# Kernel tuning notes

Measured on AMD Instinct MI355X. Metric: run time of the kernel, lower is better.

## Reference

```python
import jax, jax.numpy as jnp
import numpy as np
from jax import lax

B, T, IN, H, L, K = 2048, 192, 24, 64, 2, 20


def setup_inputs() -> dict:
    key = jax.random.key(0)
    ks = jax.random.split(key, 16)
    s = 1.0 / np.sqrt(H)

    def u(k, shape):
        return jax.random.uniform(k, shape, jnp.float32, -s, s)

    # PyTorch LSTM init + forget-gate bias filled with 1.0 (bias[n//4:n//2])
    b_ih0 = u(ks[2], (4 * H,)).at[H:2 * H].set(1.0)
    b_hh0 = u(ks[3], (4 * H,)).at[H:2 * H].set(1.0)
    b_ih1 = u(ks[6], (4 * H,)).at[H:2 * H].set(1.0)
    b_hh1 = u(ks[7], (4 * H,)).at[H:2 * H].set(1.0)
    return {
        "train_batch": jax.random.normal(ks[0], (B, T, IN), jnp.float32),
        "labels_batch": jax.random.uniform(ks[1], (B, T), jnp.float32),
        "w_ih0": u(ks[4], (4 * H, IN)), "w_hh0": u(ks[5], (4 * H, H)),
        "b_ih0": b_ih0, "b_hh0": b_hh0,
        "w_ih1": u(ks[8], (4 * H, H)), "w_hh1": u(ks[9], (4 * H, H)),
        "b_ih1": b_ih1, "b_hh1": b_hh1,
        "w_b0": u(ks[10], (1, H * L)), "bb_b0": u(ks[11], (1,)),
        "w_g": u(ks[12], (K, H * L)), "b_g": u(ks[13], (K,)),
    }


def _cell(x, h, c, w_ih, w_hh, b_ih, b_hh):
    g = x @ w_ih.T + b_ih + h @ w_hh.T + b_hh
    i, f, gg, o = jnp.split(g, 4, axis=-1)  # PyTorch gate order i,f,g,o
    c2 = jax.nn.sigmoid(f) * c + jax.nn.sigmoid(i) * jnp.tanh(gg)
    h2 = jax.nn.sigmoid(o) * jnp.tanh(c2)
    return h2, c2


def _crps(beta0, gamma, labels):
    # beta0 [T,B,1], gamma [T,B,K], labels [T,B] -> per-timestep mean CRPS [T]
    Kk = gamma.shape[-1]
    b0 = beta0[..., 0]
    sig = 1.0 / Kk
    # beta = diff of (gamma - prev)/(2*sigma), with beta[...,0] seeded by beta_0
    bp = jnp.concatenate([beta0, gamma[..., :-1]], axis=-1)
    b = (gamma - bp) / (2.0 * sig)
    b = b - jnp.concatenate([jnp.zeros_like(b[..., :1]), b[..., :-1]], axis=-1)
    b = jnp.concatenate(
        [b[..., :-1], gamma[..., -1:] - b[..., :-1].sum(-1, keepdims=True)], axis=-1)
    # left knot positions ksi = [0, 1/K, ..., (K-1)/K] (via cumsum for fidelity)
    ksi_full = jnp.cumsum(jnp.full((Kk,), sig, gamma.dtype))
    ksi = jnp.concatenate([jnp.zeros((1,), gamma.dtype), ksi_full[:-1]])
    Mkk = jnp.maximum(ksi[:, None] - ksi[None, :], 0.0) ** 2  # [K,K]
    # knot values = Q(ksi): spline quantile function at left knots
    knots = b0[..., None] * ksi + jnp.einsum('tbj,ij->tbi', b, Mkk)
    diff = labels[..., None] - knots
    al = (diff > 0).astype(gamma.dtype)
    A = (al * b).sum(-1)
    Bq = b0 - 2.0 * (al * b * ksi).sum(-1)
    C = -labels + (al * b * ksi * ksi).sum(-1)
    disc = Bq * Bq - 4.0 * A * C
    ksi_pick = ksi[jnp.argmin(jnp.abs(diff), axis=-1)]
    A_safe = jnp.where(A != 0, A, 1.0)
    B_safe = jnp.where(Bq != 0, Bq, 1.0)
    quad = (-Bq + jnp.sqrt(jnp.maximum(disc, 0.0))) / (2.0 * A_safe)
    alpha = jnp.where((A != 0) & (disc >= 0), quad,
                      jnp.where(A == 0, -C / B_safe, ksi_pick))
    c1 = labels * (2.0 * alpha - 1.0)
    c2 = b0 * (1.0 / 3.0 - alpha ** 2)
    c3 = (b / 6.0 * (1.0 - ksi) ** 4).sum(-1)
    c4 = (al * (2.0 / 3.0) * b * (alpha[..., None] - ksi) ** 3).sum(-1)
    return (c1 + c2 + c3 - c4).mean(-1)  # mean over batch, per t


def reference(train_batch, labels_batch, w_ih0, w_hh0, b_ih0, b_hh0,
              w_ih1, w_hh1, b_ih1, b_hh1, w_b0, bb_b0, w_g, b_g):
    Bb = train_batch.shape[0]
    Hh = w_hh0.shape[1]
    x_seq = jnp.transpose(train_batch, (1, 0, 2))  # [T,B,IN]
    labels = labels_batch.T                         # [T,B]
    z = jnp.zeros((Bb, Hh), train_batch.dtype)

    def step(carry, x):
        h0, c0, h1, c1 = carry
        nh0, nc0 = _cell(x, h0, c0, w_ih0, w_hh0, b_ih0, b_hh0)
        nh1, nc1 = _cell(nh0, h1, c1, w_ih1, w_hh1, b_ih1, b_hh1)
        return (nh0, nc0, nh1, nc1), jnp.stack([nh0, nh1])  # [L,B,H]

    _, hs = lax.scan(step, (z, z, z, z), x_seq)  # [T,L,B,H]
    # hidden.permute(1,2,0).reshape(B, H*L): feature layout is h-major, layer-minor
    feats = jnp.transpose(hs, (0, 2, 3, 1)).reshape(hs.shape[0], Bb, Hh * L)
    beta0 = jax.nn.softplus(feats @ w_b0.T + bb_b0)  # [T,B,1]
    gamma = jax.nn.softplus(feats @ w_g.T + b_g)     # [T,B,K]
    return _crps(beta0, gamma, labels).sum()  # sum over t of per-step mean CRPS
```

## Files before the change

### kernel.cpp

```cpp
#include <hip/hip_runtime.h>
#include <math.h>

namespace {

constexpr int TT  = 192;
constexpr int INp = 24;
constexpr int Kk  = 20;
constexpr int BB  = 8;
constexpr int NTHR = 512;

constexpr int XSTR = 2308;
constexpr int HP   = 36;
constexpr int GS   = 33;

constexpr int WSA_U = 256 * 48;
constexpr int WSB_U = 256 * 64;
constexpr int WP_U  = 21 * 64;
constexpr int WTOT  = WSA_U + WSB_U + WP_U;
constexpr size_t OFF_WSB  = 49152;
constexpr size_t OFF_WP   = 114688;
constexpr size_t OFF_PART = 120832;
constexpr size_t OFF_HIST = 131072;
constexpr size_t ROW_BYTES = (size_t)TT * 64 * 4;

using short8 = __attribute__((ext_vector_type(8))) short;
using f32x4  = __attribute__((ext_vector_type(4))) float;

__device__ __forceinline__ float sigmoidf_(float x) {
  return 1.0f / (1.0f + __expf(-x));
}
__device__ __forceinline__ float tanhf_(float x) {
  return 2.0f / (1.0f + __expf(-2.0f * x)) - 1.0f;
}
__device__ __forceinline__ float softplusf_(float x) {
  return fmaxf(x, 0.0f) + log1pf(__expf(-fabsf(x)));
}
__device__ __forceinline__ unsigned cvt_pk_bf16(float a, float b) {
  unsigned r;
  asm("v_cvt_pk_bf16_f32 %0, %1, %2" : "=v"(r) : "v"(a), "v"(b));
  return r;
}
__device__ __forceinline__ unsigned bf16rne(float x) {
  unsigned u = __float_as_uint(x);
  return (u + 0x7FFFu + ((u >> 16) & 1u)) >> 16;
}
__device__ __forceinline__ short8 as_bf(uint4 u) {
  short8 s; __builtin_memcpy(&s, &u, 16); return s;
}
#define DOT2(acc, wv, vv) \
  asm("v_dot2_f32_bf16 %0, %1, %2, %0" : "+v"(acc) : "v"(wv), "v"(vv))

#define WAVE_LDS_FENCE()                                  \
  do {                                                    \
    asm volatile("s_waitcnt lgkmcnt(0)" ::: "memory");    \
    __builtin_amdgcn_sched_barrier(0);                    \
  } while (0)

__global__ void wconv_kernel(const float* __restrict__ w_ih0,
                             const float* __restrict__ w_hh0,
                             const float* __restrict__ w_ih1,
                             const float* __restrict__ w_hh1,
                             const float* __restrict__ w_b0,
                             const float* __restrict__ w_g,
                             unsigned* __restrict__ wsA,
                             unsigned* __restrict__ wsB,
                             unsigned* __restrict__ wp) {
  int i = (int)(blockIdx.x * 256 + threadIdx.x);
  if (i >= WTOT) return;
  float lo = 0.f, hi = 0.f;
  if (i < WSA_U) {
    int g = i / 48, j = i % 48;
    int orig = (g & 3) * 64 + (g >> 2);
    if (j < 12)      { lo = w_ih0[orig * 24 + 2 * j]; hi = w_ih0[orig * 24 + 2 * j + 1]; }
    else if (j < 44) { lo = w_hh0[orig * 64 + 2 * (j - 12)]; hi = w_hh0[orig * 64 + 2 * (j - 12) + 1]; }
    wsA[i] = bf16rne(lo) | (bf16rne(hi) << 16);
  } else if (i < WSA_U + WSB_U) {
    int i2 = i - WSA_U;
    int g = i2 / 64, j = i2 % 64;
    int orig = (g & 3) * 64 + (g >> 2);
    if (j < 32) { lo = w_ih1[orig * 64 + 2 * j]; hi = w_ih1[orig * 64 + 2 * j + 1]; }
    else        { lo = w_hh1[orig * 64 + 2 * (j - 32)]; hi = w_hh1[orig * 64 + 2 * (j - 32) + 1]; }
    wsB[i2] = bf16rne(lo) | (bf16rne(hi) << 16);
  } else {
    int i3 = i - WSA_U - WSB_U;
    int o = i3 >> 6, j = i3 & 63;
    const float* row = (o == 0) ? w_b0 : (w_g + (size_t)(o - 1) * 128);
    if (j < 32) { lo = row[4 * j];            hi = row[4 * j + 2]; }
    else        { lo = row[4 * (j - 32) + 1]; hi = row[4 * (j - 32) + 3]; }
    wp[i3] = bf16rne(lo) | (bf16rne(hi) << 16);
  }
}

__global__ __launch_bounds__(NTHR, 1) void lstm_kernel(
    const float* __restrict__ train,
    const float* __restrict__ b_ih0, const float* __restrict__ b_hh0,
    const float* __restrict__ b_ih1, const float* __restrict__ b_hh1,
    const unsigned* __restrict__ wsA,
    const unsigned* __restrict__ wsB,
    unsigned* __restrict__ hist,
    int rb)
{
  __shared__ __align__(16) unsigned xpk_l[BB][XSTR];
  __shared__ __align__(16) unsigned hpk0_l[2][BB][HP];
  __shared__ __align__(16) unsigned hpk1_l[2][BB][HP];
  __shared__ float gscr_l[8][BB][GS];

  const int tid   = (int)threadIdx.x;
  const int lane  = tid & 63;
  const int w     = tid >> 6;
  const int l15   = lane & 15;
  const int grp   = lane >> 4;
  const int row_a = lane & 7;
  const int crow  = lane & 7;
  const int cfl   = lane >> 3;
  const int feat  = w * 8 + cfl;
  const int r0g   = rb + (int)blockIdx.x * BB;

  for (int i = tid; i < BB * TT * 12; i += NTHR) {
    int r = i / (TT * 12), rem = i % (TT * 12);
    int t = rem / 12, u = rem % 12;
    const float* p = train + ((size_t)(r0g + r) * TT + t) * INp + 2 * u;
    float2 v = *(const float2*)p;
    xpk_l[r][t * 12 + u] = cvt_pk_bf16(v.x, v.y);
  }
  for (int i = tid; i < 2 * BB * HP; i += NTHR) {
    (&hpk0_l[0][0][0])[i] = 0u;
    (&hpk1_l[0][0][0])[i] = 0u;
  }

  uint4 wAf[2][3], wBf[2][4];
#pragma unroll
  for (int n = 0; n < 2; ++n) {
    const int gcol = w * 32 + n * 16 + l15;
    const unsigned* pa = wsA + (size_t)gcol * 48 + grp * 4;
    wAf[n][0] = *(const uint4*)(pa);
    wAf[n][1] = *(const uint4*)(pa + 16);
    wAf[n][2] = *(const uint4*)(pa + 32);
    const unsigned* pb = wsB + (size_t)gcol * 64 + grp * 4;
#pragma unroll
    for (int c = 0; c < 4; ++c) wBf[n][c] = *(const uint4*)(pb + c * 16);
  }

  float bq0[4], bq1[4];
#pragma unroll
  for (int q = 0; q < 4; ++q) {
    bq0[q] = b_ih0[q * 64 + feat] + b_hh0[q * 64 + feat];
    bq1[q] = b_ih1[q * 64 + feat] + b_hh1[q * 64 + feat];
  }
  float c0 = 0.0f, c1 = 0.0f;

  unsigned* histp = hist + (size_t)((size_t)blockIdx.x * BB + crow) * TT * 64;
  const int j0 = w * 4 + (cfl >> 1);
  const bool writer = ((cfl & 1) == 0);

  __syncthreads();

  for (int t = 0; t < TT; ++t) {
    const int wp_ = t & 1, rp_ = wp_ ^ 1;

    {
      const unsigned* p0 = (grp < 3) ? &xpk_l[row_a][t * 12 + grp * 4]
                                     : &hpk0_l[rp_][row_a][0];
      short8 A0 = as_bf(*(const uint4*)p0);
      short8 A1 = as_bf(*(const uint4*)&hpk0_l[rp_][row_a][4 + grp * 4]);
      short8 A2 = as_bf(*(const uint4*)&hpk0_l[rp_][row_a][20 + grp * 4]);
      f32x4 acc0 = {0.f, 0.f, 0.f, 0.f};
      f32x4 acc1 = {0.f, 0.f, 0.f, 0.f};
      acc0 = __builtin_amdgcn_mfma_f32_16x16x32_bf16(A0, as_bf(wAf[0][0]), acc0, 0, 0, 0);
      acc1 = __builtin_amdgcn_mfma_f32_16x16x32_bf16(A0, as_bf(wAf[1][0]), acc1, 0, 0, 0);
      acc0 = __builtin_amdgcn_mfma_f32_16x16x32_bf16(A1, as_bf(wAf[0][1]), acc0, 0, 0, 0);
      acc1 = __builtin_amdgcn_mfma_f32_16x16x32_bf16(A1, as_bf(wAf[1][1]), acc1, 0, 0, 0);
      acc0 = __builtin_amdgcn_mfma_f32_16x16x32_bf16(A2, as_bf(wAf[0][2]), acc0, 0, 0, 0);
      acc1 = __builtin_amdgcn_mfma_f32_16x16x32_bf16(A2, as_bf(wAf[1][2]), acc1, 0, 0, 0);
      if (lane < 32) {
        const int rbse = (lane >> 4) * 4;
#pragma unroll
        for (int r = 0; r < 4; ++r) {
          gscr_l[w][rbse + r][l15]      = acc0[r];
          gscr_l[w][rbse + r][l15 + 16] = acc1[r];
        }
      }
    }
    WAVE_LDS_FENCE();
    {
      float gi_ = gscr_l[w][crow][cfl * 4 + 0] + bq0[0];
      float gf_ = gscr_l[w][crow][cfl * 4 + 1] + bq0[1];
      float gg_ = gscr_l[w][crow][cfl * 4 + 2] + bq0[2];
      float go_ = gscr_l[w][crow][cfl * 4 + 3] + bq0[3];
      float cn = sigmoidf_(gf_) * c0 + sigmoidf_(gi_) * tanhf_(gg_);
      c0 = cn;
      float h0v = sigmoidf_(go_) * tanhf_(cn);
      float hpart = __shfl_xor(h0v, 8, 64);
      if (writer) {
        unsigned pk = cvt_pk_bf16(h0v, hpart);
        hpk0_l[wp_][crow][j0] = pk;
        histp[(size_t)t * 64 + j0] = pk;
      }
    }
    __syncthreads();

    {
      short8 B0 = as_bf(*(const uint4*)&hpk0_l[wp_][row_a][grp * 4]);
      short8 B1v = as_bf(*(const uint4*)&hpk0_l[wp_][row_a][16 + grp * 4]);
      short8 B2v = as_bf(*(const uint4*)&hpk1_l[rp_][row_a][grp * 4]);
      short8 B3v = as_bf(*(const uint4*)&hpk1_l[rp_][row_a][16 + grp * 4]);
      f32x4 acc0 = {0.f, 0.f, 0.f, 0.f};
      f32x4 acc1 = {0.f, 0.f, 0.f, 0.f};
      acc0 = __builtin_amdgcn_mfma_f32_16x16x32_bf16(B0, as_bf(wBf[0][0]), acc0, 0, 0, 0);
      acc1 = __builtin_amdgcn_mfma_f32_16x16x32_bf16(B0, as_bf(wBf[1][0]), acc1, 0, 0, 0);
      acc0 = __builtin_amdgcn_mfma_f32_16x16x32_bf16(B1v, as_bf(wBf[0][1]), acc0, 0, 0, 0);
      acc1 = __builtin_amdgcn_mfma_f32_16x16x32_bf16(B1v, as_bf(wBf[1][1]), acc1, 0, 0, 0);
      acc0 = __builtin_amdgcn_mfma_f32_16x16x32_bf16(B2v, as_bf(wBf[0][2]), acc0, 0, 0, 0);
      acc1 = __builtin_amdgcn_mfma_f32_16x16x32_bf16(B2v, as_bf(wBf[1][2]), acc1, 0, 0, 0);
      acc0 = __builtin_amdgcn_mfma_f32_16x16x32_bf16(B3v, as_bf(wBf[0][3]), acc0, 0, 0, 0);
      acc1 = __builtin_amdgcn_mfma_f32_16x16x32_bf16(B3v, as_bf(wBf[1][3]), acc1, 0, 0, 0);
      if (lane < 32) {
        const int rbse = (lane >> 4) * 4;
#pragma unroll
        for (int r = 0; r < 4; ++r) {
          gscr_l[w][rbse + r][l15]      = acc0[r];
          gscr_l[w][rbse + r][l15 + 16] = acc1[r];
        }
      }
    }
    WAVE_LDS_FENCE();
    {
      float gi_ = gscr_l[w][crow][cfl * 4 + 0] + bq1[0];
      float gf_ = gscr_l[w][crow][cfl * 4 + 1] + bq1[1];
      float gg_ = gscr_l[w][crow][cfl * 4 + 2] + bq1[2];
      float go_ = gscr_l[w][crow][cfl * 4 + 3] + bq1[3];
      float cn = sigmoidf_(gf_) * c1 + sigmoidf_(gi_) * tanhf_(gg_);
      c1 = cn;
      float h1v = sigmoidf_(go_) * tanhf_(cn);
      float hpart = __shfl_xor(h1v, 8, 64);
      if (writer) {
        unsigned pk = cvt_pk_bf16(h1v, hpart);
        hpk1_l[wp_][crow][j0] = pk;
        histp[(size_t)t * 64 + 32 + j0] = pk;
      }
    }
  }
}

__global__ __launch_bounds__(192, 2) void crps_kernel(
    const unsigned* __restrict__ hist,
    const float* __restrict__ labels,
    const unsigned* __restrict__ wp,
    const float* __restrict__ bb_b0,
    const float* __restrict__ b_g,
    float* __restrict__ partials,
    int rb)
{
  __shared__ unsigned wp_l[21][64];
  __shared__ float pb_l[21];
  __shared__ float rw_l[3];

  const int tid = (int)threadIdx.x;
  const int bloc = (int)blockIdx.x;
  const int bglob = rb + bloc;
  const float sig = 1.0f / (float)Kk;

  for (int i = tid; i < 21 * 64; i += 192) wp_l[i >> 6][i & 63] = wp[i];
  if (tid < 21) pb_l[tid] = (tid == 0) ? bb_b0[0] : b_g[tid - 1];
  __syncthreads();

  uint4 hh[16];
  const uint4* hp4 = (const uint4*)(hist + ((size_t)bloc * TT + tid) * 64);
#pragma unroll
  for (int c = 0; c < 16; ++c) hh[c] = hp4[c];
  const float y = labels[(size_t)bglob * TT + tid];

  float bg[21];
#pragma unroll
  for (int o = 0; o < 21; ++o) {
    float lin = pb_l[o];
#pragma unroll
    for (int c = 0; c < 16; ++c) {
      uint4 wv = *(const uint4*)&wp_l[o][c * 4];
      DOT2(lin, wv.x, hh[c].x);
      DOT2(lin, wv.y, hh[c].y);
      DOT2(lin, wv.z, hh[c].z);
      DOT2(lin, wv.w, hh[c].w);
    }
    bg[o] = softplusf_(lin);
  }

  float braw[Kk], bj[Kk], ksi[Kk];
  {
    float kv = 0.0f;
#pragma unroll
    for (int l = 0; l < Kk; ++l) { ksi[l] = kv; kv += sig; }
  }
#pragma unroll
  for (int l = 0; l < Kk; ++l) {
    float bp = (l == 0) ? bg[0] : bg[l];
    braw[l] = (bg[l + 1] - bp) / (2.0f * sig);
  }
#pragma unroll
  for (int l = 0; l < Kk; ++l)
    bj[l] = braw[l] - ((l == 0) ? 0.0f : braw[l - 1]);
  {
    float st = 0.0f;
#pragma unroll
    for (int l = 0; l < Kk - 1; ++l) st += bj[l];
    bj[Kk - 1] = bg[Kk] - st;
  }

  float A = 0.f, tB = 0.f, tC = 0.f, c3a = 0.f;
  float ab[Kk];
  float ad = 3.4e38f, kpick = 0.f;
#pragma unroll
  for (int i = 0; i < Kk; ++i) {
    float kn = bg[0] * ksi[i];
#pragma unroll
    for (int j = 0; j < Kk; ++j) {
      if (j < i) {
        float d = ksi[i] - ksi[j];
        kn = fmaf(bj[j] * d, d, kn);
      }
    }
    float diff = y - kn;
    float abv = (diff > 0.0f) ? bj[i] : 0.0f;
    ab[i] = abv;
    A += abv;
    tB = fmaf(abv, ksi[i], tB);
    tC = fmaf(abv * ksi[i], ksi[i], tC);
    float um = 1.0f - ksi[i], um2 = um * um;
    c3a = fmaf(bj[i] * (1.0f / 6.0f), um2 * um2, c3a);
    float adi = fabsf(diff);
    if (adi < ad) { ad = adi; kpick = ksi[i]; }
  }
  float Bq = bg[0] - 2.0f * tB;
  float Cc = -y + tC;
  float disc = Bq * Bq - 4.0f * A * Cc;
  float A_safe = (A != 0.0f) ? A : 1.0f;
  float B_safe = (Bq != 0.0f) ? Bq : 1.0f;
  float quad = (-Bq + sqrtf(fmaxf(disc, 0.0f))) / (2.0f * A_safe);
  float alpha = (A != 0.0f && disc >= 0.0f)
                    ? quad
                    : ((A == 0.0f) ? (-Cc / B_safe) : kpick);
  float c4 = 0.0f;
#pragma unroll
  for (int i = 0; i < Kk; ++i) {
    float d = alpha - ksi[i];
    c4 = fmaf(ab[i] * (2.0f / 3.0f), d * d * d, c4);
  }
  float crps = y * (2.0f * alpha - 1.0f) +
               bg[0] * ((1.0f / 3.0f) - alpha * alpha) + c3a - c4;

  float v = crps;
#pragma unroll
  for (int off = 32; off > 0; off >>= 1) v += __shfl_xor(v, off, 64);
  if ((tid & 63) == 0) rw_l[tid >> 6] = v;
  __syncthreads();
  if (tid == 0) partials[bglob] = rw_l[0] + rw_l[1] + rw_l[2];
}

__global__ void final_reduce_kernel(const float* __restrict__ partials,
                                    float* __restrict__ out) {
  __shared__ float s_l[1024];
  const int tid = (int)threadIdx.x;
  s_l[tid] = partials[tid] + partials[tid + 1024];
  __syncthreads();
  for (int s = 512; s > 0; s >>= 1) {
    if (tid < s) s_l[tid] += s_l[tid + s];
    __syncthreads();
  }
  if (tid == 0) out[0] = s_l[0] * (1.0f / 2048.0f);
}

}

extern "C" void kernel_launch(void* const* d_in, const int* in_sizes, int n_in,
                              void* d_out, int out_size, void* d_ws, size_t ws_size,
                              hipStream_t stream) {
  (void)in_sizes; (void)n_in; (void)out_size;
  const float* train  = (const float*)d_in[0];
  const float* labels = (const float*)d_in[1];
  const float* w_ih0  = (const float*)d_in[2];
  const float* w_hh0  = (const float*)d_in[3];
  const float* b_ih0  = (const float*)d_in[4];
  const float* b_hh0  = (const float*)d_in[5];
  const float* w_ih1  = (const float*)d_in[6];
  const float* w_hh1  = (const float*)d_in[7];
  const float* b_ih1  = (const float*)d_in[8];
  const float* b_hh1  = (const float*)d_in[9];
  const float* w_b0   = (const float*)d_in[10];
  const float* bb_b0  = (const float*)d_in[11];
  const float* w_g    = (const float*)d_in[12];
  const float* b_g    = (const float*)d_in[13];

  unsigned* wsA   = (unsigned*)d_ws;
  unsigned* wsB   = (unsigned*)((char*)d_ws + OFF_WSB);
  unsigned* wp    = (unsigned*)((char*)d_ws + OFF_WP);
  float* partials = (float*)((char*)d_ws + OFF_PART);
  unsigned* hist  = (unsigned*)((char*)d_ws + OFF_HIST);

  size_t avail = (ws_size > OFF_HIST) ? (ws_size - OFF_HIST) : 0;
  size_t rows_fit = avail / ROW_BYTES;
  int chunk = (rows_fit >= 2048) ? 2048 : (int)rows_fit;
  chunk &= ~7;
  if (chunk < 8) chunk = 8;

  wconv_kernel<<<dim3((WTOT + 255) / 256), dim3(256), 0, stream>>>(
      w_ih0, w_hh0, w_ih1, w_hh1, w_b0, w_g, wsA, wsB, wp);

  for (int rb = 0; rb < 2048; rb += chunk) {
    int cur = (2048 - rb < chunk) ? (2048 - rb) : chunk;
    lstm_kernel<<<dim3(cur / 8), dim3(NTHR), 0, stream>>>(
        train, b_ih0, b_hh0, b_ih1, b_hh1, wsA, wsB, hist, rb);
    crps_kernel<<<dim3(cur), dim3(192), 0, stream>>>(
        hist, labels, wp, bb_b0, b_g, partials, rb);
  }
  final_reduce_kernel<<<dim3(1), dim3(1024), 0, stream>>>(partials,
                                                          (float*)d_out);
}
```

Baseline: 315.2 us.

## Split LSTM gate columns across 16 waves with one MFMA tile each

```diff
diff --git a/kernel.cpp b/kernel.cpp
--- a/kernel.cpp
+++ b/kernel.cpp
@@ -7,11 +7,11 @@
 constexpr int INp = 24;
 constexpr int Kk  = 20;
 constexpr int BB  = 8;
-constexpr int NTHR = 512;
+constexpr int NTHR = 1024;
 
 constexpr int XSTR = 2308;
 constexpr int HP   = 36;
-constexpr int GS   = 33;
+constexpr int GS   = 17;
 
 constexpr int WSA_U = 256 * 48;
 constexpr int WSB_U = 256 * 64;
@@ -53,6 +53,14 @@
 #define WAVE_LDS_FENCE()                                  \
   do {                                                    \
     asm volatile("s_waitcnt lgkmcnt(0)" ::: "memory");    \
+    __builtin_amdgcn_sched_barrier(0);                    \
+  } while (0)
+
+#define BLOCK_BARRIER_LGKM()                              \
+  do {                                                    \
+    __builtin_amdgcn_sched_barrier(0);                    \
+    asm volatile("s_waitcnt lgkmcnt(0)" ::: "memory");    \
+    __builtin_amdgcn_s_barrier();                         \
     __builtin_amdgcn_sched_barrier(0);                    \
   } while (0)
 
@@ -91,7 +99,7 @@
   }
 }
 
-__global__ __launch_bounds__(NTHR, 1) void lstm_kernel(
+__global__ __launch_bounds__(NTHR, 4) void lstm_kernel(
     const float* __restrict__ train,
     const float* __restrict__ b_ih0, const float* __restrict__ b_hh0,
     const float* __restrict__ b_ih1, const float* __restrict__ b_hh1,
@@ -103,7 +111,7 @@
   __shared__ __align__(16) unsigned xpk_l[BB][XSTR];
   __shared__ __align__(16) unsigned hpk0_l[2][BB][HP];
   __shared__ __align__(16) unsigned hpk1_l[2][BB][HP];
-  __shared__ float gscr_l[8][BB][GS];
+  __shared__ float gscr_l[16][BB][GS];
 
   const int tid   = (int)threadIdx.x;
   const int lane  = tid & 63;
@@ -112,8 +120,8 @@
   const int grp   = lane >> 4;
   const int row_a = lane & 7;
   const int crow  = lane & 7;
-  const int cfl   = lane >> 3;
-  const int feat  = w * 8 + cfl;
+  const int cfl   = (lane >> 3) & 3;
+  const int feat  = w * 4 + cfl;
   const int r0g   = rb + (int)blockIdx.x * BB;
 
   for (int i = tid; i < BB * TT * 12; i += NTHR) {
@@ -128,17 +136,16 @@
     (&hpk1_l[0][0][0])[i] = 0u;
   }
 
-  uint4 wAf[2][3], wBf[2][4];
-#pragma unroll
-  for (int n = 0; n < 2; ++n) {
-    const int gcol = w * 32 + n * 16 + l15;
+  uint4 wAf[3], wBf[4];
+  {
+    const int gcol = w * 16 + l15;
     const unsigned* pa = wsA + (size_t)gcol * 48 + grp * 4;
-    wAf[n][0] = *(const uint4*)(pa);
-    wAf[n][1] = *(const uint4*)(pa + 16);
-    wAf[n][2] = *(const uint4*)(pa + 32);
+    wAf[0] = *(const uint4*)(pa);
+    wAf[1] = *(const uint4*)(pa + 16);
+    wAf[2] = *(const uint4*)(pa + 32);
     const unsigned* pb = wsB + (size_t)gcol * 64 + grp * 4;
 #pragma unroll
-    for (int c = 0; c < 4; ++c) wBf[n][c] = *(const uint4*)(pb + c * 16);
+    for (int c = 0; c < 4; ++c) wBf[c] = *(const uint4*)(pb + c * 16);
   }
 
   float bq0[4], bq1[4];
@@ -150,8 +157,8 @@
   float c0 = 0.0f, c1 = 0.0f;
 
   unsigned* histp = hist + (size_t)((size_t)blockIdx.x * BB + crow) * TT * 64;
-  const int j0 = w * 4 + (cfl >> 1);
-  const bool writer = ((cfl & 1) == 0);
+  const int j0 = w * 2 + (cfl >> 1);
+  const bool writer = ((cfl & 1) == 0) && (lane < 32);
 
   __syncthreads();
 
@@ -164,25 +171,18 @@
       short8 A0 = as_bf(*(const uint4*)p0);
       short8 A1 = as_bf(*(const uint4*)&hpk0_l[rp_][row_a][4 + grp * 4]);
       short8 A2 = as_bf(*(const uint4*)&hpk0_l[rp_][row_a][20 + grp * 4]);
-      f32x4 acc0 = {0.f, 0.f, 0.f, 0.f};
-      f32x4 acc1 = {0.f, 0.f, 0.f, 0.f};
-      acc0 = __builtin_amdgcn_mfma_f32_16x16x32_bf16(A0, as_bf(wAf[0][0]), acc0, 0, 0, 0);
-      acc1 = __builtin_amdgcn_mfma_f32_16x16x32_bf16(A0, as_bf(wAf[1][0]), acc1, 0, 0, 0);
-      acc0 = __builtin_amdgcn_mfma_f32_16x16x32_bf16(A1, as_bf(wAf[0][1]), acc0, 0, 0, 0);
-      acc1 = __builtin_amdgcn_mfma_f32_16x16x32_bf16(A1, as_bf(wAf[1][1]), acc1, 0, 0, 0);
-      acc0 = __builtin_amdgcn_mfma_f32_16x16x32_bf16(A2, as_bf(wAf[0][2]), acc0, 0, 0, 0);
-      acc1 = __builtin_amdgcn_mfma_f32_16x16x32_bf16(A2, as_bf(wAf[1][2]), acc1, 0, 0, 0);
+      f32x4 acc = {0.f, 0.f, 0.f, 0.f};
+      acc = __builtin_amdgcn_mfma_f32_16x16x32_bf16(A0, as_bf(wAf[0]), acc, 0, 0, 0);
+      acc = __builtin_amdgcn_mfma_f32_16x16x32_bf16(A1, as_bf(wAf[1]), acc, 0, 0, 0);
+      acc = __builtin_amdgcn_mfma_f32_16x16x32_bf16(A2, as_bf(wAf[2]), acc, 0, 0, 0);
       if (lane < 32) {
         const int rbse = (lane >> 4) * 4;
 #pragma unroll
-        for (int r = 0; r < 4; ++r) {
-          gscr_l[w][rbse + r][l15]      = acc0[r];
-          gscr_l[w][rbse + r][l15 + 16] = acc1[r];
-        }
+        for (int r = 0; r < 4; ++r) gscr_l[w][rbse + r][l15] = acc[r];
       }
     }
     WAVE_LDS_FENCE();
-    {
+    if (lane < 32) {
       float gi_ = gscr_l[w][crow][cfl * 4 + 0] + bq0[0];
       float gf_ = gscr_l[w][crow][cfl * 4 + 1] + bq0[1];
       float gg_ = gscr_l[w][crow][cfl * 4 + 2] + bq0[2];
@@ -197,34 +197,26 @@
         histp[(size_t)t * 64 + j0] = pk;
       }
     }
-    __syncthreads();
+    BLOCK_BARRIER_LGKM();
 
     {
       short8 B0 = as_bf(*(const uint4*)&hpk0_l[wp_][row_a][grp * 4]);
-      short8 B1v = as_bf(*(const uint4*)&hpk0_l[wp_][row_a][16 + grp * 4]);
-      short8 B2v = as_bf(*(const uint4*)&hpk1_l[rp_][row_a][grp * 4]);
-      short8 B3v = as_bf(*(const uint4*)&hpk1_l[rp_][row_a][16 + grp * 4]);
-      f32x4 acc0 = {0.f, 0.f, 0.f, 0.f};
-      f32x4 acc1 = {0.f, 0.f, 0.f, 0.f};
-      acc0 = __builtin_amdgcn_mfma_f32_16x16x32_bf16(B0, as_bf(wBf[0][0]), acc0, 0, 0, 0);
-      acc1 = __builtin_amdgcn_mfma_f32_16x16x32_bf16(B0, as_bf(wBf[1][0]), acc1, 0, 0, 0);
-      acc0 = __builtin_amdgcn_mfma_f32_16x16x32_bf16(B1v, as_bf(wBf[0][1]), acc0, 0, 0, 0);
-      acc1 = __builtin_amdgcn_mfma_f32_16x16x32_bf16(B1v, as_bf(wBf[1][1]), acc1, 0, 0, 0);
-      acc0 = __builtin_amdgcn_mfma_f32_16x16x32_bf16(B2v, as_bf(wBf[0][2]), acc0, 0, 0, 0);
-      acc1 = __builtin_amdgcn_mfma_f32_16x16x32_bf16(B2v, as_bf(wBf[1][2]), acc1, 0, 0, 0);
-      acc0 = __builtin_amdgcn_mfma_f32_16x16x32_bf16(B3v, as_bf(wBf[0][3]), acc0, 0, 0, 0);
-      acc1 = __builtin_amdgcn_mfma_f32_16x16x32_bf16(B3v, as_bf(wBf[1][3]), acc1, 0, 0, 0);
+      short8 B1 = as_bf(*(const uint4*)&hpk0_l[wp_][row_a][16 + grp * 4]);
+      short8 B2 = as_bf(*(const uint4*)&hpk1_l[rp_][row_a][grp * 4]);
+      short8 B3 = as_bf(*(const uint4*)&hpk1_l[rp_][row_a][16 + grp * 4]);
+      f32x4 acc = {0.f, 0.f, 0.f, 0.f};
+      acc = __builtin_amdgcn_mfma_f32_16x16x32_bf16(B0, as_bf(wBf[0]), acc, 0, 0, 0);
+      acc = __builtin_amdgcn_mfma_f32_16x16x32_bf16(B1, as_bf(wBf[1]), acc, 0, 0, 0);
+      acc = __builtin_amdgcn_mfma_f32_16x16x32_bf16(B2, as_bf(wBf[2]), acc, 0, 0, 0);
+      acc = __builtin_amdgcn_mfma_f32_16x16x32_bf16(B3, as_bf(wBf[3]), acc, 0, 0, 0);
       if (lane < 32) {
         const int rbse = (lane >> 4) * 4;
 #pragma unroll
-        for (int r = 0; r < 4; ++r) {
-          gscr_l[w][rbse + r][l15]      = acc0[r];
-          gscr_l[w][rbse + r][l15 + 16] = acc1[r];
-        }
+        for (int r = 0; r < 4; ++r) gscr_l[w][rbse + r][l15] = acc[r];
       }
     }
     WAVE_LDS_FENCE();
-    {
+    if (lane < 32) {
       float gi_ = gscr_l[w][crow][cfl * 4 + 0] + bq1[0];
       float gf_ = gscr_l[w][crow][cfl * 4 + 1] + bq1[1];
       float gg_ = gscr_l[w][crow][cfl * 4 + 2] + bq1[2];
```

Result: slower. 426.3 us (+35.3%).

## Skew LSTM layers across timesteps to halve block barriers per step

Applied to the files above, without the earlier changes.

```diff
diff --git a/kernel.cpp b/kernel.cpp
--- a/kernel.cpp
+++ b/kernel.cpp
@@ -11,7 +11,7 @@
 
 constexpr int XSTR = 2308;
 constexpr int HP   = 36;
-constexpr int GS   = 33;
+constexpr int GS   = 36;
 
 constexpr int WSA_U = 256 * 48;
 constexpr int WSB_U = 256 * 64;
@@ -53,6 +53,14 @@
 #define WAVE_LDS_FENCE()                                  \
   do {                                                    \
     asm volatile("s_waitcnt lgkmcnt(0)" ::: "memory");    \
+    __builtin_amdgcn_sched_barrier(0);                    \
+  } while (0)
+
+#define BLOCK_BARRIER_LGKM()                              \
+  do {                                                    \
+    __builtin_amdgcn_sched_barrier(0);                    \
+    asm volatile("s_waitcnt lgkmcnt(0)" ::: "memory");    \
+    __builtin_amdgcn_s_barrier();                         \
     __builtin_amdgcn_sched_barrier(0);                    \
   } while (0)
 
@@ -103,7 +111,8 @@
   __shared__ __align__(16) unsigned xpk_l[BB][XSTR];
   __shared__ __align__(16) unsigned hpk0_l[2][BB][HP];
   __shared__ __align__(16) unsigned hpk1_l[2][BB][HP];
-  __shared__ float gscr_l[8][BB][GS];
+  __shared__ __align__(16) float gscrA_l[8][BB][GS];
+  __shared__ __align__(16) float gscrB_l[8][BB][GS];
 
   const int tid   = (int)threadIdx.x;
   const int lane  = tid & 63;
@@ -152,92 +161,143 @@
   unsigned* histp = hist + (size_t)((size_t)blockIdx.x * BB + crow) * TT * 64;
   const int j0 = w * 4 + (cfl >> 1);
   const bool writer = ((cfl & 1) == 0);
+  const int rbse = (lane >> 4) * 4;
 
   __syncthreads();
 
-  for (int t = 0; t < TT; ++t) {
-    const int wp_ = t & 1, rp_ = wp_ ^ 1;
+  {
+    const unsigned* p0 = (grp < 3) ? &xpk_l[row_a][grp * 4]
+                                   : &hpk0_l[1][row_a][0];
+    short8 A0 = as_bf(*(const uint4*)p0);
+    short8 A1 = as_bf(*(const uint4*)&hpk0_l[1][row_a][4 + grp * 4]);
+    short8 A2 = as_bf(*(const uint4*)&hpk0_l[1][row_a][20 + grp * 4]);
+    f32x4 z = {0.f, 0.f, 0.f, 0.f};
+    f32x4 a0 = z, a1 = z;
+    a0 = __builtin_amdgcn_mfma_f32_16x16x32_bf16(A0, as_bf(wAf[0][0]), a0, 0, 0, 0);
+    a1 = __builtin_amdgcn_mfma_f32_16x16x32_bf16(A0, as_bf(wAf[1][0]), a1, 0, 0, 0);
+    a0 = __builtin_amdgcn_mfma_f32_16x16x32_bf16(A1, as_bf(wAf[0][1]), a0, 0, 0, 0);
+    a1 = __builtin_amdgcn_mfma_f32_16x16x32_bf16(A1, as_bf(wAf[1][1]), a1, 0, 0, 0);
+    a0 = __builtin_amdgcn_mfma_f32_16x16x32_bf16(A2, as_bf(wAf[0][2]), a0, 0, 0, 0);
+    a1 = __builtin_amdgcn_mfma_f32_16x16x32_bf16(A2, as_bf(wAf[1][2]), a1, 0, 0, 0);
+    if (lane < 32) {
+#pragma unroll
+      for (int r = 0; r < 4; ++r) {
+        gscrA_l[w][rbse + r][l15]      = a0[r];
+        gscrA_l[w][rbse + r][l15 + 16] = a1[r];
+      }
+    }
+    WAVE_LDS_FENCE();
+    float4 g0v = *(const float4*)&gscrA_l[w][crow][cfl * 4];
+    float cn = sigmoidf_(g0v.y + bq0[1]) * c0 +
+               sigmoidf_(g0v.x + bq0[0]) * tanhf_(g0v.z + bq0[2]);
+    c0 = cn;
+    float h0v = sigmoidf_(g0v.w + bq0[3]) * tanhf_(cn);
+    float nb = __shfl_xor(h0v, 8, 64);
+    if (writer) {
+      unsigned pk = cvt_pk_bf16(h0v, nb);
+      hpk0_l[0][crow][j0] = pk;
+      histp[j0] = pk;
+    }
+  }
+  BLOCK_BARRIER_LGKM();
+
+  for (int i = 0; i < TT - 1; ++i) {
+    const int cur = i & 1, nxt = cur ^ 1;
+
+    short8 B0 = as_bf(*(const uint4*)&hpk0_l[cur][row_a][grp * 4]);
+    short8 B1 = as_bf(*(const uint4*)&hpk0_l[cur][row_a][16 + grp * 4]);
+    short8 B2 = as_bf(*(const uint4*)&hpk1_l[nxt][row_a][grp * 4]);
+    short8 B3 = as_bf(*(const uint4*)&hpk1_l[nxt][row_a][16 + grp * 4]);
+    const unsigned* p0 = (grp < 3) ? &xpk_l[row_a][(i + 1) * 12 + grp * 4]
+                                   : &hpk0_l[cur][row_a][0];
+    short8 A0 = as_bf(*(const uint4*)p0);
+    short8 A1 = as_bf(*(const uint4*)&hpk0_l[cur][row_a][4 + grp * 4]);
+    short8 A2 = as_bf(*(const uint4*)&hpk0_l[cur][row_a][20 + grp * 4]);
+
+    f32x4 z = {0.f, 0.f, 0.f, 0.f};
+    f32x4 b0a = z, b1a = z, a0a = z, a1a = z;
+    b0a = __builtin_amdgcn_mfma_f32_16x16x32_bf16(B0, as_bf(wBf[0][0]), b0a, 0, 0, 0);
+    b1a = __builtin_amdgcn_mfma_f32_16x16x32_bf16(B0, as_bf(wBf[1][0]), b1a, 0, 0, 0);
+    a0a = __builtin_amdgcn_mfma_f32_16x16x32_bf16(A0, as_bf(wAf[0][0]), a0a, 0, 0, 0);
+    a1a = __builtin_amdgcn_mfma_f32_16x16x32_bf16(A0, as_bf(wAf[1][0]), a1a, 0, 0, 0);
+    b0a = __builtin_amdgcn_mfma_f32_16x16x32_bf16(B1, as_bf(wBf[0][1]), b0a, 0, 0, 0);
+    b1a = __builtin_amdgcn_mfma_f32_16x16x32_bf16(B1, as_bf(wBf[1][1]), b1a, 0, 0, 0);
+    a0a = __builtin_amdgcn_mfma_f32_16x16x32_bf16(A1, as_bf(wAf[0][1]), a0a, 0, 0, 0);
+    a1a = __builtin_amdgcn_mfma_f32_16x16x32_bf16(A1, as_bf(wAf[1][1]), a1a, 0, 0, 0);
+    b0a = __builtin_amdgcn_mfma_f32_16x16x32_bf16(B2, as_bf(wBf[0][2]), b0a, 0, 0, 0);
+    b1a = __builtin_amdgcn_mfma_f32_16x16x32_bf16(B2, as_bf(wBf[1][2]), b1a, 0, 0, 0);
+    a0a = __builtin_amdgcn_mfma_f32_16x16x32_bf16(A2, as_bf(wAf[0][2]), a0a, 0, 0, 0);
+    a1a = __builtin_amdgcn_mfma_f32_16x16x32_bf16(A2, as_bf(wAf[1][2]), a1a, 0, 0, 0);
+    b0a = __builtin_amdgcn_mfma_f32_16x16x32_bf16(B3, as_bf(wBf[0][3]), b0a, 0, 0, 0);
+    b1a = __builtin_amdgcn_mfma_f32_16x16x32_bf16(B3, as_bf(wBf[1][3]), b1a, 0, 0, 0);
+
+    if (lane < 32) {
+#pragma unroll
+      for (int r = 0; r < 4; ++r) {
+        gscrB_l[w][rbse + r][l15]      = b0a[r];
+        gscrB_l[w][rbse + r][l15 + 16] = b1a[r];
+        gscrA_l[w][rbse + r][l15]      = a0a[r];
+        gscrA_l[w][rbse + r][l15 + 16] = a1a[r];
+      }
+    }
+    WAVE_LDS_FENCE();
 
     {
-      const unsigned* p0 = (grp < 3) ? &xpk_l[row_a][t * 12 + grp * 4]
-                                     : &hpk0_l[rp_][row_a][0];
-      short8 A0 = as_bf(*(const uint4*)p0);
-      short8 A1 = as_bf(*(const uint4*)&hpk0_l[rp_][row_a][4 + grp * 4]);
-      short8 A2 = as_bf(*(const uint4*)&hpk0_l[rp_][row_a][20 + grp * 4]);
-      f32x4 acc0 = {0.f, 0.f, 0.f, 0.f};
-      f32x4 acc1 = {0.f, 0.f, 0.f, 0.f};
-      acc0 = __builtin_amdgcn_mfma_f32_16x16x32_bf16(A0, as_bf(wAf[0][0]), acc0, 0, 0, 0);
-      acc1 = __builtin_amdgcn_mfma_f32_16x16x32_bf16(A0, as_bf(wAf[1][0]), acc1, 0, 0, 0);
-      acc0 = __builtin_amdgcn_mfma_f32_16x16x32_bf16(A1, as_bf(wAf[0][1]), acc0, 0, 0, 0);
-      acc1 = __builtin_amdgcn_mfma_f32_16x16x32_bf16(A1, as_bf(wAf[1][1]), acc1, 0, 0, 0);
-      acc0 = __builtin_amdgcn_mfma_f32_16x16x32_bf16(A2, as_bf(wAf[0][2]), acc0, 0, 0, 0);
-      acc1 = __builtin_amdgcn_mfma_f32_16x16x32_bf16(A2, as_bf(wAf[1][2]), acc1, 0, 0, 0);
-      if (lane < 32) {
-        const int rbse = (lane >> 4) * 4;
-#pragma unroll
-        for (int r = 0; r < 4; ++r) {
-          gscr_l[w][rbse + r][l15]      = acc0[r];
-          gscr_l[w][rbse + r][l15 + 16] = acc1[r];
-        }
+      float4 g1v = *(const float4*)&gscrB_l[w][crow][cfl * 4];
+      float4 g0v = *(const float4*)&gscrA_l[w][crow][cfl * 4];
+      float cn1 = sigmoidf_(g1v.y + bq1[1]) * c1 +
+                  sigmoidf_(g1v.x + bq1[0]) * tanhf_(g1v.z + bq1[2]);
+      c1 = cn1;
+      float h1v = sigmoidf_(g1v.w + bq1[3]) * tanhf_(cn1);
+      float cn0 = sigmoidf_(g0v.y + bq0[1]) * c0 +
+                  sigmoidf_(g0v.x + bq0[0]) * tanhf_(g0v.z + bq0[2]);
+      c0 = cn0;
+      float h0v = sigmoidf_(g0v.w + bq0[3]) * tanhf_(cn0);
+      float n1 = __shfl_xor(h1v, 8, 64);
+      float n0 = __shfl_xor(h0v, 8, 64);
+      if (writer) {
+        unsigned pk1 = cvt_pk_bf16(h1v, n1);
+        unsigned pk0 = cvt_pk_bf16(h0v, n0);
+        hpk1_l[cur][crow][j0] = pk1;
+        hpk0_l[nxt][crow][j0] = pk0;
+        histp[(size_t)i * 64 + 32 + j0] = pk1;
+        histp[(size_t)(i + 1) * 64 + j0] = pk0;
       }
     }
+    BLOCK_BARRIER_LGKM();
+  }
+
+  {
+    const int cur = (TT - 1) & 1, nxt = cur ^ 1;
+    short8 B0 = as_bf(*(const uint4*)&hpk0_l[cur][row_a][grp * 4]);
+    short8 B1 = as_bf(*(const uint4*)&hpk0_l[cur][row_a][16 + grp * 4]);
+    short8 B2 = as_bf(*(const uint4*)&hpk1_l[nxt][row_a][grp * 4]);
+    short8 B3 = as_bf(*(const uint4*)&hpk1_l[nxt][row_a][16 + grp * 4]);
+    f32x4 z = {0.f, 0.f, 0.f, 0.f};
+    f32x4 b0a = z, b1a = z;
+    b0a = __builtin_amdgcn_mfma_f32_16x16x32_bf16(B0, as_bf(wBf[0][0]), b0a, 0, 0, 0);
+    b1a = __builtin_amdgcn_mfma_f32_16x16x32_bf16(B0, as_bf(wBf[1][0]), b1a, 0, 0, 0);
+    b0a = __builtin_amdgcn_mfma_f32_16x16x32_bf16(B1, as_bf(wBf[0][1]), b0a, 0, 0, 0);
+    b1a = __builtin_amdgcn_mfma_f32_16x16x32_bf16(B1, as_bf(wBf[1][1]), b1a, 0, 0, 0);
+    b0a = __builtin_amdgcn_mfma_f32_16x16x32_bf16(B2, as_bf(wBf[0][2]), b0a, 0, 0, 0);
+    b1a = __builtin_amdgcn_mfma_f32_16x16x32_bf16(B2, as_bf(wBf[1][2]), b1a, 0, 0, 0);
+    b0a = __builtin_amdgcn_mfma_f32_16x16x32_bf16(B3, as_bf(wBf[0][3]), b0a, 0, 0, 0);
+    b1a = __builtin_amdgcn_mfma_f32_16x16x32_bf16(B3, as_bf(wBf[1][3]), b1a, 0, 0, 0);
+    if (lane < 32) {
+#pragma unroll
+      for (int r = 0; r < 4; ++r) {
+        gscrB_l[w][rbse + r][l15]      = b0a[r];
+        gscrB_l[w][rbse + r][l15 + 16] = b1a[r];
+      }
+    }
     WAVE_LDS_FENCE();
-    {
-      float gi_ = gscr_l[w][crow][cfl * 4 + 0] + bq0[0];
-      float gf_ = gscr_l[w][crow][cfl * 4 + 1] + bq0[1];
-      float gg_ = gscr_l[w][crow][cfl * 4 + 2] + bq0[2];
-      float go_ = gscr_l[w][crow][cfl * 4 + 3] + bq0[3];
-      float cn = sigmoidf_(gf_) * c0 + sigmoidf_(gi_) * tanhf_(gg_);
-      c0 = cn;
-      float h0v = sigmoidf_(go_) * tanhf_(cn);
-      float hpart = __shfl_xor(h0v, 8, 64);
-      if (writer) {
-        unsigned pk = cvt_pk_bf16(h0v, hpart);
-        hpk0_l[wp_][crow][j0] = pk;
-        histp[(size_t)t * 64 + j0] = pk;
-      }
-    }
-    __syncthreads();
-
-    {
-      short8 B0 = as_bf(*(const uint4*)&hpk0_l[wp_][row_a][grp * 4]);
-      short8 B1v = as_bf(*(const uint4*)&hpk0_l[wp_][row_a][16 + grp * 4]);
-      short8 B2v = as_bf(*(const uint4*)&hpk1_l[rp_][row_a][grp * 4]);
-      short8 B3v = as_bf(*(const uint4*)&hpk1_l[rp_][row_a][16 + grp * 4]);
-      f32x4 acc0 = {0.f, 0.f, 0.f, 0.f};
-      f32x4 acc1 = {0.f, 0.f, 0.f, 0.f};
-      acc0 = __builtin_amdgcn_mfma_f32_16x16x32_bf16(B0, as_bf(wBf[0][0]), acc0, 0, 0, 0);
-      acc1 = __builtin_amdgcn_mfma_f32_16x16x32_bf16(B0, as_bf(wBf[1][0]), acc1, 0, 0, 0);
-      acc0 = __builtin_amdgcn_mfma_f32_16x16x32_bf16(B1v, as_bf(wBf[0][1]), acc0, 0, 0, 0);
-      acc1 = __builtin_amdgcn_mfma_f32_16x16x32_bf16(B1v, as_bf(wBf[1][1]), acc1, 0, 0, 0);
-      acc0 = __builtin_amdgcn_mfma_f32_16x16x32_bf16(B2v, as_bf(wBf[0][2]), acc0, 0, 0, 0);
-      acc1 = __builtin_amdgcn_mfma_f32_16x16x32_bf16(B2v, as_bf(wBf[1][2]), acc1, 0, 0, 0);
-      acc0 = __builtin_amdgcn_mfma_f32_16x16x32_bf16(B3v, as_bf(wBf[0][3]), acc0, 0, 0, 0);
-      acc1 = __builtin_amdgcn_mfma_f32_16x16x32_bf16(B3v, as_bf(wBf[1][3]), acc1, 0, 0, 0);
-      if (lane < 32) {
-        const int rbse = (lane >> 4) * 4;
-#pragma unroll
-        for (int r = 0; r < 4; ++r) {
-          gscr_l[w][rbse + r][l15]      = acc0[r];
-          gscr_l[w][rbse + r][l15 + 16] = acc1[r];
-        }
-      }
-    }
-    WAVE_LDS_FENCE();
-    {
-      float gi_ = gscr_l[w][crow][cfl * 4 + 0] + bq1[0];
-      float gf_ = gscr_l[w][crow][cfl * 4 + 1] + bq1[1];
-      float gg_ = gscr_l[w][crow][cfl * 4 + 2] + bq1[2];
-      float go_ = gscr_l[w][crow][cfl * 4 + 3] + bq1[3];
-      float cn = sigmoidf_(gf_) * c1 + sigmoidf_(gi_) * tanhf_(gg_);
-      c1 = cn;
-      float h1v = sigmoidf_(go_) * tanhf_(cn);
-      float hpart = __shfl_xor(h1v, 8, 64);
-      if (writer) {
-        unsigned pk = cvt_pk_bf16(h1v, hpart);
-        hpk1_l[wp_][crow][j0] = pk;
-        histp[(size_t)t * 64 + 32 + j0] = pk;
-      }
+    float4 g1v = *(const float4*)&gscrB_l[w][crow][cfl * 4];
+    float cn1 = sigmoidf_(g1v.y + bq1[1]) * c1 +
+                sigmoidf_(g1v.x + bq1[0]) * tanhf_(g1v.z + bq1[2]);
+    float h1v = sigmoidf_(g1v.w + bq1[3]) * tanhf_(cn1);
+    float n1 = __shfl_xor(h1v, 8, 64);
+    if (writer) {
+      histp[(size_t)(TT - 1) * 64 + 32 + j0] = cvt_pk_bf16(h1v, n1);
     }
   }
 }
```

Measured after the change: 314.1 us. Within noise of the previous version (-0.4%).
